# Optimization experiments

Hardware: AMD Instinct MI355X
Metric: run time of the kernel (lower is better)

## Reference

```python
import jax, jax.numpy as jnp
import numpy as np

NUM_HEADS = 2
LN_EPS = 1e-5
NEG_MASK = -1e9


def setup_inputs() -> dict:
    key = jax.random.key(0)
    ks = jax.random.split(key, 8)
    B, C, T, N = 8, 64, 32, 400
    H, D = NUM_HEADS, C // NUM_HEADS
    s = 1.0 / np.sqrt(C)
    return {
        "x": jax.random.normal(ks[0], (B, C, T, N), dtype=jnp.float32),
        "Wq": jax.random.normal(ks[1], (C, C), dtype=jnp.float32) * s,
        "Wk": jax.random.normal(ks[2], (C, C), dtype=jnp.float32) * s,
        "Wv": jax.random.normal(ks[3], (C, C), dtype=jnp.float32) * s,
        "a_src": jax.random.normal(ks[4], (H, D), dtype=jnp.float32) * 0.1,
        "a_dst": jax.random.normal(ks[5], (H, D), dtype=jnp.float32) * 0.1,
        "ln_gamma": jnp.ones((C,), dtype=jnp.float32),
        "ln_beta": jnp.zeros((C,), dtype=jnp.float32),
        "gso": jax.random.randint(ks[6], (N, N), 0, 2, dtype=jnp.int32),
    }


def reference(x, Wq, Wk, Wv, a_src, a_dst, ln_gamma, ln_beta, gso):
    B, C, T, N = x.shape
    H = NUM_HEADS
    D = C // H
    # (B,C,T,N) -> (B*T, N, C)
    xr = jnp.transpose(x, (0, 2, 3, 1)).reshape(B * T, N, C)
    # torch Linear: y = x @ W.T; then split heads -> (BT, N, H, D)
    Q = (xr @ Wq.T).reshape(B * T, N, H, D)
    K = (xr @ Wk.T).reshape(B * T, N, H, D)
    V = (xr @ Wv.T).reshape(B * T, N, H, D)
    # GAT additive scores per head
    s_src = jnp.einsum("bnhd,hd->bnh", Q, a_src)  # (BT, N, H)
    s_dst = jnp.einsum("bnhd,hd->bnh", K, a_dst)  # (BT, N, H)
    scores = s_src[:, :, None, :] + s_dst[:, None, :, :]  # (BT, i, j, H)
    scores = jax.nn.leaky_relu(scores, negative_slope=0.2)
    mask = jnp.where(gso == 0, jnp.float32(NEG_MASK), 0.0)  # (N, N)
    scores = scores + mask[None, :, :, None]
    attn = jax.nn.softmax(scores, axis=2)  # softmax over dst j; dropout = identity (eval)
    out = jnp.einsum("bijh,bjhd->bihd", attn, V).reshape(B * T, N, C)
    # LayerNorm over channel dim
    mu = jnp.mean(out, axis=-1, keepdims=True)
    var = jnp.var(out, axis=-1, keepdims=True)
    out = (out - mu) * jax.lax.rsqrt(var + LN_EPS) * ln_gamma + ln_beta
    # (BT, N, C) -> (B, C, T, N)
    return jnp.transpose(out.reshape(B, T, N, C), (0, 3, 1, 2))
```

## Files before the change

### kernel.cpp

```cpp
#include <hip/hip_runtime.h>
#include <hip/hip_bf16.h>

typedef __attribute__((ext_vector_type(8))) short bf16x8;
typedef __attribute__((ext_vector_type(4))) float f32x4;
typedef __attribute__((ext_vector_type(4))) int i32x4;
typedef __attribute__((ext_vector_type(4))) unsigned int u32x4;

#define B_   8
#define C_   64
#define T_   32
#define N_   400
#define BT_  256
#define NKT_ 13
#define CN_  12800
#define VROW 424
#define WROW 72
#define L2E_ 1.4426950408889634f
#define C2_  (-13.849872392533959f)
#define SH12_ (-17.312340490667560f)

#if __has_builtin(__builtin_amdgcn_exp2f)
#define EXP2F(x) __builtin_amdgcn_exp2f(x)
#else
#define EXP2F(x) __expf((x) * 0.6931471805599453f)
#endif

__global__ __launch_bounds__(256) void gat_prep(
    const int* __restrict__ gso, unsigned int* __restrict__ mb)
{
  int idx = blockIdx.x*256 + threadIdx.x;
  if (idx < N_*16) {
    int i = idx >> 4, kw = idx & 15;
    unsigned int bits = 0;
    if (kw < 13) {
      int j0 = kw * 32;
      #pragma unroll
      for (int bb = 0; bb < 32; ++bb) {
        int j = j0 + bb;
        if (j < N_ && gso[i*N_ + j] != 0) bits |= (1u << bb);
      }
    }
    mb[idx] = bits;
  }
}

__global__ __launch_bounds__(1024) void gat_fused(
    const float* __restrict__ x, const float* __restrict__ Wq,
    const float* __restrict__ Wk, const float* __restrict__ Wv,
    const float* __restrict__ a_src, const float* __restrict__ a_dst,
    const float* __restrict__ gamma, const float* __restrict__ beta,
    const unsigned int* __restrict__ mb, float* __restrict__ out)
{
  __shared__ __align__(16) __hip_bfloat16 Vt[64][VROW];
  __shared__ __align__(16) __hip_bfloat16 wvb[80][WROW];
  __shared__ __align__(16) float sd_s[2][416];
  __shared__ __align__(16) float si_s[2][400];
  __shared__ __align__(16) float ob[128][68];
  __shared__ float g_s[64], b_s[64];

  const int tid = threadIdx.x;
  const int bt = blockIdx.x;
  const int b = bt >> 5, t = bt & 31;
  const int lane = tid & 63, wave = tid >> 6;
  const int col = lane & 15, quad = lane >> 4;

  #pragma unroll
  for (int it = 0; it < 4; ++it) {
    int idx = it*1024 + tid;
    int o = idx >> 6, c = idx & 63;
    wvb[o][c] = __float2bfloat16(Wv[o*C_ + c]);
  }
  if (tid < 256) {
    int ww = tid >> 6, c = tid & 63, h = ww >> 1;
    const float* W = (ww & 1) ? Wk : Wq;
    const float* a = (ww & 1) ? a_dst : a_src;
    float s = 0.f;
    #pragma unroll
    for (int d = 0; d < 32; ++d) s += W[(h*32 + d)*C_ + c] * a[h*32 + d];
    wvb[64 + ww][c] = __float2bfloat16(s * L2E_);
  } else if (tid < 320) {
    g_s[tid - 256] = gamma[tid - 256];
  } else if (tid < 384) {
    b_s[tid - 320] = beta[tid - 320];
  } else if (tid < 416) {
    int tt = tid - 384;
    sd_s[tt >> 4][400 + (tt & 15)] = 0.f;
  }
  for (int idx = tid; idx < 12*WROW; idx += 1024)
    wvb[68 + idx/WROW][idx % WROW] = __float2bfloat16(0.f);
  for (int idx = tid; idx < 64*24; idx += 1024)
    Vt[idx/24][400 + idx%24] = __float2bfloat16(0.f);
  __syncthreads();

  {
    const float* xbase = x + ((size_t)b*C_*T_ + t)*N_;
    for (int nt = wave; nt < 25; nt += 16) {
      const int n0 = nt*16;
      bf16x8 bfrag[2];
      #pragma unroll
      for (int kt = 0; kt < 2; ++kt) {
        const float* xc = xbase + (size_t)(kt*32 + quad*8)*CN_ + n0 + col;
        union { short s[8]; bf16x8 v; } pk;
        #pragma unroll
        for (int j = 0; j < 8; ++j) {
          union { __hip_bfloat16 h; short s; } cv;
          cv.h = __float2bfloat16(xc[(size_t)j*CN_]);
          pk.s[j] = cv.s;
        }
        bfrag[kt] = pk.v;
      }
      #pragma unroll
      for (int ot = 0; ot < 5; ++ot) {
        f32x4 acc = {0.f, 0.f, 0.f, 0.f};
        #pragma unroll
        for (int kt = 0; kt < 2; ++kt) {
          bf16x8 afr = *(const bf16x8*)&wvb[ot*16 + col][kt*32 + quad*8];
          acc = __builtin_amdgcn_mfma_f32_16x16x32_bf16(afr, bfrag[kt], acc, 0, 0, 0);
        }
        if (ot < 4) {
          #pragma unroll
          for (int r = 0; r < 4; ++r)
            Vt[ot*16 + quad*4 + r][n0 + col] = __float2bfloat16(acc[r]);
        } else if (quad == 0) {
          #pragma unroll
          for (int r = 0; r < 4; ++r) {
            int h = r >> 1;
            if (r & 1) sd_s[h][n0 + col] = acc[r];
            else       si_s[h][n0 + col] = acc[r] + SH12_;
          }
        }
      }
    }
  }
  __syncthreads();

  const int hh = wave & 1, itile = wave >> 1;
  const int rowA = col;

  bf16x8 ones;
  #pragma unroll
  for (int k = 0; k < 8; ++k) ones[k] = (short)0x3F80;

  for (int r0 = 0; r0 < N_; r0 += 128) {
    const int ibase = r0 + itile*16;
    if (ibase < N_) {
      const int irow = ibase + rowA;
      const float si1 = si_s[hh][irow];
      const u32x4* mp = (const u32x4*)(mb + irow*16);
      u32x4 mw0 = mp[0], mw1 = mp[1], mw2 = mp[2];
      unsigned int mw12 = mb[irow*16 + 12];
      const float* sdp = sd_s[hh] + quad*8;
      const __hip_bfloat16* v0p = &Vt[hh*32 + rowA][quad*8];
      const __hip_bfloat16* v1p = v0p + 16*VROW;

      f32x4 d0 = {0,0,0,0}, d1 = {0,0,0,0}, d2 = {0,0,0,0};
      #pragma unroll
      for (int kt = 0; kt < NKT_; ++kt) {
        unsigned int mword = (kt < 4) ? mw0[kt] : (kt < 8) ? mw1[kt-4]
                           : (kt < 12) ? mw2[kt-8] : mw12;
        unsigned int mbyte = (mword >> (quad*8)) & 0xffu;
        f32x4 s0 = *(const f32x4*)(sdp + kt*32);
        f32x4 s1 = *(const f32x4*)(sdp + kt*32 + 4);
        bf16x8 vb0 = *(const bf16x8*)(v0p + kt*32);
        bf16x8 vb1 = *(const bf16x8*)(v1p + kt*32);
        int em[8];
        #pragma unroll
        for (int jj = 0; jj < 8; ++jj) {
          float sd = (jj < 4) ? s0[jj] : s1[jj-4];
          float t1 = si1 + sd;
          float t2 = fmaf(0.2f, t1, C2_);
          float v  = fmaxf(t1, t2);
          float e  = EXP2F(v);
          int msk = ((int)(mbyte << (31 - jj))) >> 31;
          em[jj] = __float_as_int(e) & msk;
        }
        union { i32x4 i; bf16x8 v; } af;
        af.i.x = (int)__builtin_amdgcn_perm((unsigned)em[1], (unsigned)em[0], 0x07060302u);
        af.i.y = (int)__builtin_amdgcn_perm((unsigned)em[3], (unsigned)em[2], 0x07060302u);
        af.i.z = (int)__builtin_amdgcn_perm((unsigned)em[5], (unsigned)em[4], 0x07060302u);
        af.i.w = (int)__builtin_amdgcn_perm((unsigned)em[7], (unsigned)em[6], 0x07060302u);
        d0 = __builtin_amdgcn_mfma_f32_16x16x32_bf16(af.v, vb0, d0, 0, 0, 0);
        d1 = __builtin_amdgcn_mfma_f32_16x16x32_bf16(af.v, vb1, d1, 0, 0, 0);
        d2 = __builtin_amdgcn_mfma_f32_16x16x32_bf16(af.v, ones, d2, 0, 0, 0);
      }
      #pragma unroll
      for (int r = 0; r < 4; ++r) {
        float li = 1.0f / d2[r];
        int rl = itile*16 + quad*4 + r;
        ob[rl][hh*32 + rowA]      = d0[r] * li;
        ob[rl][hh*32 + 16 + rowA] = d1[r] * li;
      }
    }
    __syncthreads();

    {
      int rl = tid >> 3, cgi = tid & 7;
      int n = r0 + rl;
      if (n < N_) {
        float u[8]; float s = 0.f;
        #pragma unroll
        for (int k = 0; k < 8; ++k) { u[k] = ob[rl][cgi*8 + k]; s += u[k]; }
        s += __shfl_xor(s,1); s += __shfl_xor(s,2); s += __shfl_xor(s,4);
        float mu = s * (1.f/64.f);
        float q = 0.f;
        #pragma unroll
        for (int k = 0; k < 8; ++k) { float dv = u[k]-mu; q = fmaf(dv,dv,q); }
        q += __shfl_xor(q,1); q += __shfl_xor(q,2); q += __shfl_xor(q,4);
        float rstd = rsqrtf(q*(1.f/64.f) + 1e-5f);
        #pragma unroll
        for (int k = 0; k < 8; ++k)
          ob[rl][cgi*8 + k] = (u[k]-mu)*rstd*g_s[cgi*8 + k] + b_s[cgi*8 + k];
      }
    }
    __syncthreads();

    #pragma unroll
    for (int it = 0; it < 8; ++it) {
      int idx = it*1024 + tid;
      int c = idx >> 7, nn = idx & 127;
      int n = r0 + nn;
      if (n < N_) out[((size_t)(b*C_ + c)*T_ + t)*N_ + n] = ob[nn][c];
    }
    __syncthreads();
  }
}

extern "C" void kernel_launch(void* const* d_in, const int* in_sizes, int n_in,
                              void* d_out, int out_size, void* d_ws, size_t ws_size,
                              hipStream_t stream) {
  (void)in_sizes; (void)n_in; (void)out_size; (void)ws_size;
  const float* x     = (const float*)d_in[0];
  const float* Wq    = (const float*)d_in[1];
  const float* Wk    = (const float*)d_in[2];
  const float* Wv    = (const float*)d_in[3];
  const float* a_src = (const float*)d_in[4];
  const float* a_dst = (const float*)d_in[5];
  const float* gamma = (const float*)d_in[6];
  const float* beta  = (const float*)d_in[7];
  const int*   gso   = (const int*)d_in[8];
  float* out = (float*)d_out;

  unsigned int* mb = (unsigned int*)d_ws;

  gat_prep<<<26, 256, 0, stream>>>(gso, mb);
  gat_fused<<<BT_, 1024, 0, stream>>>(x, Wq, Wk, Wv, a_src, a_dst,
                                      gamma, beta, mb, out);
}
```

Measured before the change: 122.7 us.

## Factor leaky-relu exponent into per-row and per-column exp products

Rewrites exp2(leaky_relu(si+sd)) as max(E1i*e1d, E2i*e2d). The per-column exponentials are precomputed once in shared memory and the per-row ones once per row, so the inner attention loop does two multiplies and a max instead of an add, fma, max and exp per element. Masking now uses a small shared-memory lookup table that ANDs packed bf16 pairs, replacing per-element shift masks. The cost is twice as many shared-memory loads for the column terms plus the LUT loads, and products of exponentials risk overflow or underflow, which the reduced shift constant is meant to limit.

Result: faster. 115.9 us (median of 2 runs) (-5.5%).

```diff
diff --git a/kernel.cpp b/kernel.cpp
--- a/kernel.cpp
+++ b/kernel.cpp
@@ -5,6 +5,7 @@
 typedef __attribute__((ext_vector_type(4))) float f32x4;
 typedef __attribute__((ext_vector_type(4))) int i32x4;
 typedef __attribute__((ext_vector_type(4))) unsigned int u32x4;
+typedef __attribute__((ext_vector_type(2))) unsigned int u32x2;
 
 #define B_   8
 #define C_   64
@@ -16,8 +17,7 @@
 #define VROW 424
 #define WROW 72
 #define L2E_ 1.4426950408889634f
-#define C2_  (-13.849872392533959f)
-#define SH12_ (-17.312340490667560f)
+#define SH6_ (-8.656170245333780f)
 
 #if __has_builtin(__builtin_amdgcn_exp2f)
 #define EXP2F(x) __builtin_amdgcn_exp2f(x)
@@ -53,9 +53,11 @@
 {
   __shared__ __align__(16) __hip_bfloat16 Vt[64][VROW];
   __shared__ __align__(16) __hip_bfloat16 wvb[80][WROW];
-  __shared__ __align__(16) float sd_s[2][416];
+  __shared__ __align__(16) float e1d_s[2][416];
+  __shared__ __align__(16) float e2d_s[2][416];
   __shared__ __align__(16) float si_s[2][400];
   __shared__ __align__(16) float ob[128][68];
+  __shared__ __align__(16) unsigned int lut_s[16][2];
   __shared__ float g_s[64], b_s[64];
 
   const int tid = threadIdx.x;
@@ -82,9 +84,14 @@
     g_s[tid - 256] = gamma[tid - 256];
   } else if (tid < 384) {
     b_s[tid - 320] = beta[tid - 320];
-  } else if (tid < 416) {
+  } else if (tid < 448) {
     int tt = tid - 384;
-    sd_s[tt >> 4][400 + (tt & 15)] = 0.f;
+    int h = (tt >> 4) & 1, cc = 400 + (tt & 15);
+    if (tt < 32) e1d_s[h][cc] = 0.f; else e2d_s[h][cc] = 0.f;
+  } else if (tid < 464) {
+    int n = tid - 448;
+    lut_s[n][0] = ((n & 1) ? 0x0000FFFFu : 0u) | ((n & 2) ? 0xFFFF0000u : 0u);
+    lut_s[n][1] = ((n & 4) ? 0x0000FFFFu : 0u) | ((n & 8) ? 0xFFFF0000u : 0u);
   }
   for (int idx = tid; idx < 12*WROW; idx += 1024)
     wvb[68 + idx/WROW][idx % WROW] = __float2bfloat16(0.f);
@@ -125,8 +132,12 @@
           #pragma unroll
           for (int r = 0; r < 4; ++r) {
             int h = r >> 1;
-            if (r & 1) sd_s[h][n0 + col] = acc[r];
-            else       si_s[h][n0 + col] = acc[r] + SH12_;
+            if (r & 1) {
+              e1d_s[h][n0 + col] = EXP2F(acc[r] + SH6_);
+              e2d_s[h][n0 + col] = EXP2F(fmaf(0.2f, acc[r], SH6_));
+            } else {
+              si_s[h][n0 + col] = acc[r];
+            }
           }
         }
       }
@@ -136,6 +147,7 @@
 
   const int hh = wave & 1, itile = wave >> 1;
   const int rowA = col;
+  const unsigned int qsh = quad * 8;
 
   bf16x8 ones;
   #pragma unroll
@@ -146,10 +158,13 @@
     if (ibase < N_) {
       const int irow = ibase + rowA;
       const float si1 = si_s[hh][irow];
+      const float E1i = EXP2F(si1 + SH6_);
+      const float E2i = EXP2F(fmaf(0.2f, si1, SH6_));
       const u32x4* mp = (const u32x4*)(mb + irow*16);
       u32x4 mw0 = mp[0], mw1 = mp[1], mw2 = mp[2];
       unsigned int mw12 = mb[irow*16 + 12];
-      const float* sdp = sd_s[hh] + quad*8;
+      const float* e1p = e1d_s[hh] + quad*8;
+      const float* e2p = e2d_s[hh] + quad*8;
       const __hip_bfloat16* v0p = &Vt[hh*32 + rowA][quad*8];
       const __hip_bfloat16* v1p = v0p + 16*VROW;
 
@@ -158,27 +173,27 @@
       for (int kt = 0; kt < NKT_; ++kt) {
         unsigned int mword = (kt < 4) ? mw0[kt] : (kt < 8) ? mw1[kt-4]
                            : (kt < 12) ? mw2[kt-8] : mw12;
-        unsigned int mbyte = (mword >> (quad*8)) & 0xffu;
-        f32x4 s0 = *(const f32x4*)(sdp + kt*32);
-        f32x4 s1 = *(const f32x4*)(sdp + kt*32 + 4);
+        unsigned int mbyte = (mword >> qsh) & 0xffu;
+        u32x2 mlo = *(const u32x2*)&lut_s[mbyte & 15u][0];
+        u32x2 mhi = *(const u32x2*)&lut_s[mbyte >> 4][0];
+        f32x4 x1a = *(const f32x4*)(e1p + kt*32);
+        f32x4 x1b = *(const f32x4*)(e1p + kt*32 + 4);
+        f32x4 x2a = *(const f32x4*)(e2p + kt*32);
+        f32x4 x2b = *(const f32x4*)(e2p + kt*32 + 4);
         bf16x8 vb0 = *(const bf16x8*)(v0p + kt*32);
         bf16x8 vb1 = *(const bf16x8*)(v1p + kt*32);
-        int em[8];
+        unsigned int eu[8];
         #pragma unroll
         for (int jj = 0; jj < 8; ++jj) {
-          float sd = (jj < 4) ? s0[jj] : s1[jj-4];
-          float t1 = si1 + sd;
-          float t2 = fmaf(0.2f, t1, C2_);
-          float v  = fmaxf(t1, t2);
-          float e  = EXP2F(v);
-          int msk = ((int)(mbyte << (31 - jj))) >> 31;
-          em[jj] = __float_as_int(e) & msk;
+          float f1 = (jj < 4) ? x1a[jj] : x1b[jj-4];
+          float f2 = (jj < 4) ? x2a[jj] : x2b[jj-4];
+          eu[jj] = __float_as_uint(fmaxf(E1i * f1, E2i * f2));
         }
         union { i32x4 i; bf16x8 v; } af;
-        af.i.x = (int)__builtin_amdgcn_perm((unsigned)em[1], (unsigned)em[0], 0x07060302u);
-        af.i.y = (int)__builtin_amdgcn_perm((unsigned)em[3], (unsigned)em[2], 0x07060302u);
-        af.i.z = (int)__builtin_amdgcn_perm((unsigned)em[5], (unsigned)em[4], 0x07060302u);
-        af.i.w = (int)__builtin_amdgcn_perm((unsigned)em[7], (unsigned)em[6], 0x07060302u);
+        af.i.x = (int)(__builtin_amdgcn_perm(eu[1], eu[0], 0x07060302u) & mlo.x);
+        af.i.y = (int)(__builtin_amdgcn_perm(eu[3], eu[2], 0x07060302u) & mlo.y);
+        af.i.z = (int)(__builtin_amdgcn_perm(eu[5], eu[4], 0x07060302u) & mhi.x);
+        af.i.w = (int)(__builtin_amdgcn_perm(eu[7], eu[6], 0x07060302u) & mhi.y);
         d0 = __builtin_amdgcn_mfma_f32_16x16x32_bf16(af.v, vb0, d0, 0, 0, 0);
         d1 = __builtin_amdgcn_mfma_f32_16x16x32_bf16(af.v, vb1, d1, 0, 0, 0);
         d2 = __builtin_amdgcn_mfma_f32_16x16x32_bf16(af.v, ones, d2, 0, 0, 0);
@@ -240,9 +255,9 @@
   const int*   gso   = (const int*)d_in[8];
   float* out = (float*)d_out;
 
-  unsigned int* mb = (unsigned int*)d_ws;
-
-  gat_prep<<<26, 256, 0, stream>>>(gso, mb);
+  unsigned int* mbp = (unsigned int*)d_ws;
+
+  gat_prep<<<26, 256, 0, stream>>>(gso, mbp);
   gat_fused<<<BT_, 1024, 0, stream>>>(x, Wq, Wk, Wv, a_src, a_dst,
-                                      gamma, beta, mb, out);
+                                      gamma, beta, mbp, out);
 }
```
